# Optimization experiments

Hardware: AMD Instinct MI355X
Metric: run time of the kernel (lower is better)

Reference implementation:

```python
import jax, jax.numpy as jnp
import numpy as np

K_NEIGHBORS = 16  # matches init kwarg k


def _knn_idx(x, K):
    # x: (b, n, 3). Full pairwise squared distances, then top-K smallest.
    sq = jnp.sum(x * x, axis=-1)                                   # (b, n)
    d2 = sq[:, :, None] + sq[:, None, :] - 2.0 * jnp.einsum('bnc,bmc->bnm', x, x)
    _, idx = jax.lax.top_k(-d2, K)                                  # nearest first (includes self)
    return idx                                                      # (b, n, K)


def _gather(points, idx):
    # points: (b, n, C), idx: (b, n, K) -> (b, n, K, C)
    return jax.vmap(lambda p, i: p[i])(points, idx)


def _kappa_std(pc, normal, k):
    # pc, normal: (b, 3, n)
    x = pc.transpose(0, 2, 1)        # (b, n, 3)
    nrm = normal.transpose(0, 2, 1)  # (b, n, 3)
    idx = _knn_idx(x, k + 1)         # (b, n, k+1)
    nn_pts = _gather(x, idx)[:, :, 1:, :]          # drop self -> (b, n, k, 3)
    v = nn_pts - x[:, :, None, :]                   # (b, n, k, 3)
    v = v / jnp.clip(jnp.linalg.norm(v, axis=-1, keepdims=True), 1e-12)
    kappa = jnp.abs(jnp.sum(v * nrm[:, :, None, :], axis=-1)).mean(axis=-1)  # (b, n)
    nn_kappa = _gather(kappa[..., None], idx)[:, :, 1:, 0]                    # (b, n, k)
    # torch.std default: unbiased (ddof=1)
    return jnp.std(nn_kappa, axis=-1, ddof=1)                                  # (b, n)


def setup_inputs() -> dict:
    key = jax.random.key(0)
    k1, k2, k3 = jax.random.split(key, 3)
    b, n = 4, 4096
    ori_data = jax.random.normal(k1, (b, 3, n), dtype=jnp.float32)
    adv_data = ori_data + 0.05 * jax.random.normal(k2, (b, 3, n), dtype=jnp.float32)
    nrm = jax.random.normal(k3, (b, 3, n), dtype=jnp.float32)
    ori_normal = nrm / jnp.clip(jnp.linalg.norm(nrm, axis=1, keepdims=True), 1e-12)
    return {"ori_data": ori_data, "adv_data": adv_data, "ori_normal": ori_normal}


def reference(ori_data, adv_data, ori_normal):
    k = K_NEIGHBORS
    ori_std = _kappa_std(ori_data, ori_normal, k)   # (b, n)
    adv_std = _kappa_std(adv_data, ori_normal, k)   # (b, n)
    # torch PairwiseDistance(p=2, eps=1e-6): ||x1 - x2 + eps||_2 over last dim
    dist = jnp.linalg.norm(ori_std - adv_std + 1e-6, axis=-1)  # (b,)
    return dist.mean()
```

## Files before the change

kernel.cpp:

```cpp
#include <hip/hip_runtime.h>
#include <math.h>

#define NPTS 4096
#define BATCH 4
#define KNB 16
#define BIG 3.0e38f
#define CAP 512

__device__ __forceinline__ void bsort_stage(float& d, int& s, int lane, int k, int j) {
  const float od = __shfl_xor(d, j);
  const int   os = __shfl_xor(s, j);
  const bool keepMin = ((lane & k) == 0) == ((lane & j) == 0);
  const bool takeO = keepMin ? (od < d) : (od > d);
  d = takeO ? od : d;
  s = takeO ? os : s;
}

__device__ __forceinline__ void bitonic_sort64(float& d, int& s, int lane) {
#pragma unroll
  for (int k = 2; k <= 64; k <<= 1) {
#pragma unroll
    for (int j = k >> 1; j >= 1; j >>= 1)
      bsort_stage(d, s, lane, k, j);
  }
}

__device__ __forceinline__ void bitonic_merge64(float& d, int& s, int lane) {
#pragma unroll
  for (int j = 32; j >= 1; j >>= 1)
    bsort_stage(d, s, lane, 64, j);
}

__global__ __launch_bounds__(256)
void knn_kappa_kernel(const float* __restrict__ ori,
                      const float* __restrict__ adv,
                      const float* __restrict__ nrm,
                      float* __restrict__ kappaWs,
                      int* __restrict__ idxWs,
                      float* __restrict__ accum) {
  const int i    = blockIdx.x;
  const int b    = blockIdx.y;
  const int ds   = blockIdx.z;
  const int t    = threadIdx.x;
  const int lane = t & 63;
  const int w    = t >> 6;

  if (i == 0 && b == 0 && ds == 0 && t < 8) accum[t] = 0.0f;

  const float* __restrict__ P = (ds == 0 ? ori : adv) + (size_t)b * 3 * NPTS;
  const float4* __restrict__ X4 = (const float4*)(P);
  const float4* __restrict__ Y4 = (const float4*)(P + NPTS);
  const float4* __restrict__ Z4 = (const float4*)(P + 2 * NPTS);

  __shared__ float candD[CAP];
  __shared__ int   candI[CAP];
  __shared__ unsigned int wTau[4];
  __shared__ unsigned int cnt;

  if (t == 0) cnt = 0;

  const float xi = P[i], yi = P[NPTS + i], zi = P[2 * NPTS + i];

  float d[16];
  float tmin = BIG;
  const int base4 = t * 4;
#pragma unroll
  for (int k = 0; k < 4; ++k) {
    const float4 xv = X4[base4 + k];
    const float4 yv = Y4[base4 + k];
    const float4 zv = Z4[base4 + k];
    {
      const float dx = xv.x - xi, dy = yv.x - yi, dz = zv.x - zi;
      d[k * 4 + 0] = fmaf(dx, dx, fmaf(dy, dy, dz * dz));
    }
    {
      const float dx = xv.y - xi, dy = yv.y - yi, dz = zv.y - zi;
      d[k * 4 + 1] = fmaf(dx, dx, fmaf(dy, dy, dz * dz));
    }
    {
      const float dx = xv.z - xi, dy = yv.z - yi, dz = zv.z - zi;
      d[k * 4 + 2] = fmaf(dx, dx, fmaf(dy, dy, dz * dz));
    }
    {
      const float dx = xv.w - xi, dy = yv.w - yi, dz = zv.w - zi;
      d[k * 4 + 3] = fmaf(dx, dx, fmaf(dy, dy, dz * dz));
    }
    tmin = fminf(tmin, fminf(fminf(d[k * 4 + 0], d[k * 4 + 1]),
                             fminf(d[k * 4 + 2], d[k * 4 + 3])));
  }

  {
    const unsigned mb = __float_as_uint(tmin);
    unsigned G = 0;
#pragma unroll
    for (int bit = 11; bit >= 0; --bit) {
      const unsigned trial = G | (1u << bit);
      const unsigned T = (trial << 19) | 0x7FFFFu;
      const int c = __popcll(__ballot(mb <= T));
      if (c < 17) G = trial;
    }
    unsigned T0 = (G << 19) | 0x7FFFFu;
    const int c0 = __popcll(__ballot(mb <= T0));
    if (c0 < 17) T0 = ((G + 1u) << 19) | 0x7FFFFu;
    if (lane == 0) wTau[w] = T0;
  }
  __syncthreads();
  const unsigned tauBits = min(min(wTau[0], wTau[1]), min(wTau[2], wTau[3]));

#pragma unroll
  for (int u = 0; u < 16; ++u) {
    if (__float_as_uint(d[u]) <= tauBits) {
      const unsigned pos = atomicAdd(&cnt, 1u);
      if (pos < CAP) { candD[pos] = d[u]; candI[pos] = t * 16 + u; }
    }
  }
  __syncthreads();

  if (w == 0) {
    const int M = (int)(cnt < CAP ? cnt : CAP);
    float sd = (lane < M) ? candD[lane] : BIG;
    int   si = (lane < M) ? lane : -1;
    bitonic_sort64(sd, si, lane);
    for (int c0 = 64; c0 < M; c0 += 64) {
      const int slot = c0 + lane;
      float vd = (slot < M) ? candD[slot] : BIG;
      int   vi = (slot < M) ? slot : -1;
      bitonic_sort64(vd, vi, lane);
      const float rd = __shfl_xor(vd, 63);
      const int   ri = __shfl_xor(vi, 63);
      if (rd < sd) { sd = rd; si = ri; }
      bitonic_merge64(sd, si, lane);
    }

    const int siN = __shfl(si, lane + 1);
    if (lane < KNB) {
      const int nbj = candI[siN];
      const float vx = P[nbj] - xi;
      const float vy = P[NPTS + nbj] - yi;
      const float vz = P[2 * NPTS + nbj] - zi;
      float L = fmaxf(sqrtf(fmaf(vx, vx, fmaf(vy, vy, vz * vz))), 1e-12f);
      const float* __restrict__ nb_ = nrm + (size_t)b * 3 * NPTS;
      const float nx = nb_[i], ny = nb_[NPTS + i], nz = nb_[2 * NPTS + i];
      float c = fabsf(fmaf(vx, nx, fmaf(vy, ny, vz * nz)) / L);
      c += __shfl_xor(c, 1);
      c += __shfl_xor(c, 2);
      c += __shfl_xor(c, 4);
      c += __shfl_xor(c, 8);
      const size_t row = (size_t)(ds * BATCH + b) * NPTS + i;
      if (lane == 0) kappaWs[row] = c * (1.0f / 16.0f);
      idxWs[row * KNB + lane] = nbj;
    }
  }
}

__global__ __launch_bounds__(256)
void std_dist_kernel(const float* __restrict__ kappaWs,
                     const int* __restrict__ idxWs,
                     float* __restrict__ accum,
                     float* __restrict__ out) {
  const int i = blockIdx.x * 256 + threadIdx.x;
  const int b = blockIdx.y;

  float s[2];
#pragma unroll
  for (int ds = 0; ds < 2; ++ds) {
    const size_t kb = (size_t)(ds * BATCH + b) * NPTS;
    const int4* __restrict__ ip = (const int4*)(idxWs + (kb + i) * KNB);
    const int4 q0 = ip[0], q1 = ip[1], q2 = ip[2], q3 = ip[3];
    const float* __restrict__ kp = kappaWs + kb;
    float kv[16];
    kv[0] = kp[q0.x];  kv[1] = kp[q0.y];  kv[2] = kp[q0.z];  kv[3] = kp[q0.w];
    kv[4] = kp[q1.x];  kv[5] = kp[q1.y];  kv[6] = kp[q1.z];  kv[7] = kp[q1.w];
    kv[8] = kp[q2.x];  kv[9] = kp[q2.y];  kv[10] = kp[q2.z]; kv[11] = kp[q2.w];
    kv[12] = kp[q3.x]; kv[13] = kp[q3.y]; kv[14] = kp[q3.z]; kv[15] = kp[q3.w];
    float sum = 0.f;
#pragma unroll
    for (int u = 0; u < 16; ++u) sum += kv[u];
    const float mean = sum * (1.0f / 16.0f);
    float ss = 0.f;
#pragma unroll
    for (int u = 0; u < 16; ++u) {
      const float dv = kv[u] - mean;
      ss = fmaf(dv, dv, ss);
    }
    s[ds] = sqrtf(ss * (1.0f / 15.0f));
  }

  float dq = s[0] - s[1] + 1e-6f;
  dq = dq * dq;

  dq += __shfl_xor(dq, 32);
  dq += __shfl_xor(dq, 16);
  dq += __shfl_xor(dq, 8);
  dq += __shfl_xor(dq, 4);
  dq += __shfl_xor(dq, 2);
  dq += __shfl_xor(dq, 1);
  __shared__ float red[4];
  if ((threadIdx.x & 63) == 0) red[threadIdx.x >> 6] = dq;
  __syncthreads();

  if (threadIdx.x == 0) {
    const float blockSum = red[0] + red[1] + red[2] + red[3];
    atomicAdd(&accum[b], blockSum);
    __threadfence();
    const unsigned old = atomicAdd((unsigned int*)(accum + 4), 1u);
    if (old == 63) {
      float ssum = 0.f;
#pragma unroll
      for (int bb = 0; bb < 4; ++bb) ssum += sqrtf(atomicAdd(&accum[bb], 0.0f));
      out[0] = ssum * 0.25f;
    }
  }
}

extern "C" void kernel_launch(void* const* d_in, const int* in_sizes, int n_in,
                              void* d_out, int out_size, void* d_ws, size_t ws_size,
                              hipStream_t stream) {
  const float* ori = (const float*)d_in[0];
  const float* adv = (const float*)d_in[1];
  const float* nrm = (const float*)d_in[2];
  float* out = (float*)d_out;

  float* kappaWs = (float*)d_ws;
  int*   idxWs   = (int*)((char*)d_ws + (size_t)2 * BATCH * NPTS * 4);
  float* accum   = (float*)((char*)d_ws + (size_t)2 * BATCH * NPTS * 4
                                        + (size_t)2 * BATCH * NPTS * KNB * 4);

  dim3 g1(NPTS, BATCH, 2);
  knn_kappa_kernel<<<g1, 256, 0, stream>>>(ori, adv, nrm, kappaWs, idxWs, accum);

  dim3 g2(NPTS / 256, BATCH);
  std_dist_kernel<<<g2, 256, 0, stream>>>(kappaWs, idxWs, accum, out);
}
```

Baseline: 157.4 us.

## Process eight query points per block reusing register-cached candidate coordinates

Each block now handles eight query points instead of one. The 4096 candidate coordinates are loaded into registers once per block and reused across all eight queries, which cuts global load traffic and the block count by a factor of eight. The final sort and kappa work is spread so each of the four waves handles two queries, instead of only wave 0 working while the others sit idle. The candidate buffer capacity per query shrinks to 256, and the serial query loop adds a barrier per query and more shared memory per block.

```diff
diff --git a/kernel.cpp b/kernel.cpp
--- a/kernel.cpp
+++ b/kernel.cpp
@@ -4,8 +4,9 @@
 #define NPTS 4096
 #define BATCH 4
 #define KNB 16
+#define QB 8
+#define CAP 256
 #define BIG 3.0e38f
-#define CAP 512
 
 __device__ __forceinline__ void bsort_stage(float& d, int& s, int lane, int k, int j) {
   const float od = __shfl_xor(d, j);
@@ -38,92 +39,103 @@
                       float* __restrict__ kappaWs,
                       int* __restrict__ idxWs,
                       float* __restrict__ accum) {
-  const int i    = blockIdx.x;
+  const int blk  = blockIdx.x;
   const int b    = blockIdx.y;
   const int ds   = blockIdx.z;
   const int t    = threadIdx.x;
   const int lane = t & 63;
   const int w    = t >> 6;
-
-  if (i == 0 && b == 0 && ds == 0 && t < 8) accum[t] = 0.0f;
+  const int i0   = blk * QB;
+
+  if (blk == 0 && b == 0 && ds == 0 && t < 8) accum[t] = 0.0f;
 
   const float* __restrict__ P = (ds == 0 ? ori : adv) + (size_t)b * 3 * NPTS;
+
+  __shared__ float qx[QB], qy[QB], qz[QB];
+  __shared__ unsigned wTau[QB][4];
+  __shared__ unsigned cnt[QB];
+  __shared__ float candD[QB][CAP];
+  __shared__ int   candI[QB][CAP];
+
+  if (t < QB) {
+    cnt[t] = 0;
+    qx[t] = P[i0 + t];
+    qy[t] = P[NPTS + i0 + t];
+    qz[t] = P[2 * NPTS + i0 + t];
+  }
+
   const float4* __restrict__ X4 = (const float4*)(P);
   const float4* __restrict__ Y4 = (const float4*)(P + NPTS);
   const float4* __restrict__ Z4 = (const float4*)(P + 2 * NPTS);
-
-  __shared__ float candD[CAP];
-  __shared__ int   candI[CAP];
-  __shared__ unsigned int wTau[4];
-  __shared__ unsigned int cnt;
-
-  if (t == 0) cnt = 0;
-
-  const float xi = P[i], yi = P[NPTS + i], zi = P[2 * NPTS + i];
-
-  float d[16];
-  float tmin = BIG;
-  const int base4 = t * 4;
+  float cx[16], cy[16], cz[16];
 #pragma unroll
   for (int k = 0; k < 4; ++k) {
-    const float4 xv = X4[base4 + k];
-    const float4 yv = Y4[base4 + k];
-    const float4 zv = Z4[base4 + k];
+    const float4 xv = X4[t * 4 + k];
+    const float4 yv = Y4[t * 4 + k];
+    const float4 zv = Z4[t * 4 + k];
+    cx[k*4+0]=xv.x; cx[k*4+1]=xv.y; cx[k*4+2]=xv.z; cx[k*4+3]=xv.w;
+    cy[k*4+0]=yv.x; cy[k*4+1]=yv.y; cy[k*4+2]=yv.z; cy[k*4+3]=yv.w;
+    cz[k*4+0]=zv.x; cz[k*4+1]=zv.y; cz[k*4+2]=zv.z; cz[k*4+3]=zv.w;
+  }
+  __syncthreads();
+
+  for (int q = 0; q < QB; ++q) {
+    const float xi = qx[q], yi = qy[q], zi = qz[q];
+    float d[16];
+    float tmin = BIG;
+#pragma unroll
+    for (int u = 0; u < 16; ++u) {
+      const float dx = cx[u] - xi;
+      const float dy = cy[u] - yi;
+      const float dz = cz[u] - zi;
+      d[u] = fmaf(dx, dx, fmaf(dy, dy, dz * dz));
+      tmin = fminf(tmin, d[u]);
+    }
+
     {
-      const float dx = xv.x - xi, dy = yv.x - yi, dz = zv.x - zi;
-      d[k * 4 + 0] = fmaf(dx, dx, fmaf(dy, dy, dz * dz));
-    }
-    {
-      const float dx = xv.y - xi, dy = yv.y - yi, dz = zv.y - zi;
-      d[k * 4 + 1] = fmaf(dx, dx, fmaf(dy, dy, dz * dz));
-    }
-    {
-      const float dx = xv.z - xi, dy = yv.z - yi, dz = zv.z - zi;
-      d[k * 4 + 2] = fmaf(dx, dx, fmaf(dy, dy, dz * dz));
-    }
-    {
-      const float dx = xv.w - xi, dy = yv.w - yi, dz = zv.w - zi;
-      d[k * 4 + 3] = fmaf(dx, dx, fmaf(dy, dy, dz * dz));
-    }
-    tmin = fminf(tmin, fminf(fminf(d[k * 4 + 0], d[k * 4 + 1]),
-                             fminf(d[k * 4 + 2], d[k * 4 + 3])));
-  }
-
-  {
-    const unsigned mb = __float_as_uint(tmin);
-    unsigned G = 0;
-#pragma unroll
-    for (int bit = 11; bit >= 0; --bit) {
-      const unsigned trial = G | (1u << bit);
-      const unsigned T = (trial << 19) | 0x7FFFFu;
-      const int c = __popcll(__ballot(mb <= T));
-      if (c < 17) G = trial;
-    }
-    unsigned T0 = (G << 19) | 0x7FFFFu;
-    const int c0 = __popcll(__ballot(mb <= T0));
-    if (c0 < 17) T0 = ((G + 1u) << 19) | 0x7FFFFu;
-    if (lane == 0) wTau[w] = T0;
+      const unsigned mb = __float_as_uint(tmin);
+      unsigned G = 0;
+#pragma unroll
+      for (int bit = 11; bit >= 0; --bit) {
+        const unsigned trial = G | (1u << bit);
+        const unsigned T = (trial << 19) | 0x7FFFFu;
+        const int c = __popcll(__ballot(mb <= T));
+        if (c < 17) G = trial;
+      }
+      unsigned T0 = (G << 19) | 0x7FFFFu;
+      const int c0 = __popcll(__ballot(mb <= T0));
+      if (c0 < 17) T0 = ((G + 1u) << 19) | 0x7FFFFu;
+      if (lane == 0) wTau[q][w] = T0;
+    }
+    __syncthreads();
+    const unsigned tb = min(min(wTau[q][0], wTau[q][1]),
+                            min(wTau[q][2], wTau[q][3]));
+
+#pragma unroll
+    for (int u = 0; u < 16; ++u) {
+      if (__float_as_uint(d[u]) <= tb) {
+        const unsigned pos = atomicAdd(&cnt[q], 1u);
+        if (pos < CAP) {
+          candD[q][pos] = d[u];
+          candI[q][pos] = t * 16 + u;
+        }
+      }
+    }
   }
   __syncthreads();
-  const unsigned tauBits = min(min(wTau[0], wTau[1]), min(wTau[2], wTau[3]));
-
-#pragma unroll
-  for (int u = 0; u < 16; ++u) {
-    if (__float_as_uint(d[u]) <= tauBits) {
-      const unsigned pos = atomicAdd(&cnt, 1u);
-      if (pos < CAP) { candD[pos] = d[u]; candI[pos] = t * 16 + u; }
-    }
-  }
-  __syncthreads();
-
-  if (w == 0) {
-    const int M = (int)(cnt < CAP ? cnt : CAP);
-    float sd = (lane < M) ? candD[lane] : BIG;
+
+#pragma unroll
+  for (int s = 0; s < 2; ++s) {
+    const int q  = w * 2 + s;
+    const int qi = i0 + q;
+    const int M  = (int)(cnt[q] < CAP ? cnt[q] : CAP);
+
+    float sd = (lane < M) ? candD[q][lane] : BIG;
     int   si = (lane < M) ? lane : -1;
     bitonic_sort64(sd, si, lane);
     for (int c0 = 64; c0 < M; c0 += 64) {
       const int slot = c0 + lane;
-      float vd = (slot < M) ? candD[slot] : BIG;
+      float vd = (slot < M) ? candD[q][slot] : BIG;
       int   vi = (slot < M) ? slot : -1;
       bitonic_sort64(vd, vi, lane);
       const float rd = __shfl_xor(vd, 63);
@@ -134,19 +146,20 @@
 
     const int siN = __shfl(si, lane + 1);
     if (lane < KNB) {
-      const int nbj = candI[siN];
+      const int nbj = candI[q][siN];
+      const float xi = qx[q], yi = qy[q], zi = qz[q];
       const float vx = P[nbj] - xi;
       const float vy = P[NPTS + nbj] - yi;
       const float vz = P[2 * NPTS + nbj] - zi;
-      float L = fmaxf(sqrtf(fmaf(vx, vx, fmaf(vy, vy, vz * vz))), 1e-12f);
+      const float L = fmaxf(sqrtf(fmaf(vx, vx, fmaf(vy, vy, vz * vz))), 1e-12f);
       const float* __restrict__ nb_ = nrm + (size_t)b * 3 * NPTS;
-      const float nx = nb_[i], ny = nb_[NPTS + i], nz = nb_[2 * NPTS + i];
+      const float nx = nb_[qi], ny = nb_[NPTS + qi], nz = nb_[2 * NPTS + qi];
       float c = fabsf(fmaf(vx, nx, fmaf(vy, ny, vz * nz)) / L);
       c += __shfl_xor(c, 1);
       c += __shfl_xor(c, 2);
       c += __shfl_xor(c, 4);
       c += __shfl_xor(c, 8);
-      const size_t row = (size_t)(ds * BATCH + b) * NPTS + i;
+      const size_t row = (size_t)(ds * BATCH + b) * NPTS + qi;
       if (lane == 0) kappaWs[row] = c * (1.0f / 16.0f);
       idxWs[row * KNB + lane] = nbj;
     }
@@ -226,7 +239,7 @@
   float* accum   = (float*)((char*)d_ws + (size_t)2 * BATCH * NPTS * 4
                                         + (size_t)2 * BATCH * NPTS * KNB * 4);
 
-  dim3 g1(NPTS, BATCH, 2);
+  dim3 g1(NPTS / QB, BATCH, 2);
   knn_kappa_kernel<<<g1, 256, 0, stream>>>(ori, adv, nrm, kappaWs, idxWs, accum);
 
   dim3 g2(NPTS / 256, BATCH);
```

Result: no change. 154.3 us (-1.9%).
